# Performance work log

Measured on AMD Instinct MI355X. Metric: run time of the kernel, lower is better.

## Reference

```python
import jax, jax.numpy as jnp
import numpy as np

EPS = 1e-7


def setup_inputs() -> dict:
    key = jax.random.key(0)
    k1, k2, k3 = jax.random.split(key, 3)
    B, Nt, Nv, D = 64, 128, 256, 512
    text_feats = jax.random.normal(k1, (B, Nt, D), dtype=jnp.float32)
    visual_feats = jax.random.normal(k2, (B, Nv, D), dtype=jnp.float32)
    attention_mask = jax.random.randint(k3, (B, Nt), 0, 2, dtype=jnp.int32)
    return {"text_feats": text_feats, "visual_feats": visual_feats,
            "attention_mask": attention_mask}


def _l2norm(x):
    return x / jnp.clip(jnp.linalg.norm(x, axis=-1, keepdims=True), 1e-12)


def reference(text_feats, visual_feats, attention_mask):
    # Normalize token features (F.normalize along D)
    t = _l2norm(text_feats)            # (B, Nt, D)
    v = _l2norm(visual_feats)          # (B, Nv, D)
    # All-pairs token similarities: (B, B, Nt, Nv)
    token_sims = jnp.einsum('itd,jvd->ijtv', t, v)
    # Max over visual tokens -> (B, B, Nt)
    max_sims = jnp.max(token_sims, axis=3)
    # Masked mean over text tokens -> (B, B)
    mask = attention_mask.astype(jnp.float32)[:, None, :]   # (B, 1, Nt) broadcasts over pairs
    masked_sum = jnp.sum(max_sims * mask, axis=2)            # (B, B)
    valid = jnp.clip(jnp.sum(mask, axis=2), EPS)             # (B, 1)
    clip_sims = masked_sum / valid                           # (B, B)
    # Symmetric InfoNCE on the diagonal
    B = clip_sims.shape[0]
    diag = jnp.arange(B)
    losses_t2v = -jax.nn.log_softmax(clip_sims, axis=1)[diag, diag]
    losses_v2t = -jax.nn.log_softmax(clip_sims.T, axis=1)[diag, diag]
    contrastive_loss = jnp.mean(losses_t2v + losses_v2t) / 2.0
    # Regularization: keep negative token sims near zero
    neg_sims = jnp.clip(token_sims, -20.0, 0.0)
    reg_loss = 0.15 * jnp.mean(neg_sims ** 2)
    return contrastive_loss + reg_loss
```

## Files before the change

### kernel.cpp

```cpp
#include <hip/hip_runtime.h>
#include <hip/hip_bf16.h>

#define BB 64
#define NT 128
#define NV 256
#define DD 512
#define BKB 128
#define EPSF 1e-7f

typedef __attribute__((ext_vector_type(8))) int i32x8;
typedef __attribute__((ext_vector_type(4))) int i32x4;
typedef __attribute__((ext_vector_type(4))) float f32x4;

__device__ __forceinline__ void glds16(const uchar* g, uchar* l) {
    __builtin_amdgcn_global_load_lds(
        (const __attribute__((address_space(1))) unsigned int*)g,
        (__attribute__((address_space(3))) unsigned int*)l, 16, 0, 0);
}

__global__ __launch_bounds__(256) void k_normalize(
    const float* __restrict__ tf, const float* __restrict__ vf,
    uchar* __restrict__ tn, uchar* __restrict__ vn,
    float* __restrict__ reg_sum) {
    if (blockIdx.x == 0 && threadIdx.x == 0) *reg_sum = 0.0f;
    const int w = threadIdx.x >> 6, l = threadIdx.x & 63;
    const int row = blockIdx.x * 4 + w;
    const float* src;
    uchar* dst;
    if (row < BB * NT) {
        src = tf + (size_t)row * DD;
        dst = tn + (size_t)row * DD;
    } else {
        int r = row - BB * NT;
        src = vf + (size_t)r * DD;
        dst = vn + (size_t)r * DD;
    }
    float4 x0 = ((const float4*)src)[l * 2];
    float4 x1 = ((const float4*)src)[l * 2 + 1];
    float ss = x0.x * x0.x + x0.y * x0.y + x0.z * x0.z + x0.w * x0.w
             + x1.x * x1.x + x1.y * x1.y + x1.z * x1.z + x1.w * x1.w;
    #pragma unroll
    for (int off = 32; off; off >>= 1) ss += __shfl_xor(ss, off, 64);
    float scale = 1.0f / fmaxf(sqrtf(ss), 1e-12f);
    int p0 = __builtin_amdgcn_cvt_pk_fp8_f32(x0.x * scale, x0.y * scale, 0, 0);
    p0 = __builtin_amdgcn_cvt_pk_fp8_f32(x0.z * scale, x0.w * scale, p0, 1);
    int p1 = __builtin_amdgcn_cvt_pk_fp8_f32(x1.x * scale, x1.y * scale, 0, 0);
    p1 = __builtin_amdgcn_cvt_pk_fp8_f32(x1.z * scale, x1.w * scale, p1, 1);
    ((uint2*)dst)[l] = make_uint2((unsigned)p0, (unsigned)p1);
}

__global__ __launch_bounds__(512, 2) void k_gemm(
    const uchar* __restrict__ tn, const uchar* __restrict__ vn,
    const int* __restrict__ mask,
    float* __restrict__ clip_sims, float* __restrict__ reg_sum) {
    __shared__ uchar sT0[NT * BKB];
    __shared__ uchar sT1[NT * BKB];
    __shared__ uchar sV0[NV * BKB];
    __shared__ uchar sV1[NV * BKB];
    __shared__ float maxbuf[NT][4];
    __shared__ float redw[8];
    __shared__ float c0[2], c1[2];

    const int i = blockIdx.x, j = blockIdx.y;
    const int tid = threadIdx.x;
    const int l = tid & 63, w = tid >> 6;
    const int wr = w >> 2, wc = w & 3;
    const int m15 = l & 15, q = l >> 4;

    const uchar* tbase = tn + (size_t)i * NT * DD;
    const uchar* vbase = vn + (size_t)j * NV * DD;

    int t_off[2], v_off[4];
    #pragma unroll
    for (int s = 0; s < 2; ++s) {
        int f = s * 512 + tid;
        int r = f >> 3, p = f & 7, g = (p - r) & 7;
        t_off[s] = r * DD + g * 16;
    }
    #pragma unroll
    for (int s = 0; s < 4; ++s) {
        int f = s * 512 + tid;
        int r = f >> 3, p = f & 7, g = (p - r) & 7;
        v_off[s] = r * DD + g * 16;
    }

    int a_b0[4], a_b1[4], b_b0[4], b_b1[4];
    #pragma unroll
    for (int rt = 0; rt < 4; ++rt) {
        int row = wr * 64 + rt * 16 + m15;
        a_b0[rt] = row * BKB + (((2 * q + row) & 7) * 16);
        a_b1[rt] = row * BKB + (((2 * q + 1 + row) & 7) * 16);
    }
    #pragma unroll
    for (int ct = 0; ct < 4; ++ct) {
        int row = wc * 64 + ct * 16 + m15;
        b_b0[ct] = row * BKB + (((2 * q + row) & 7) * 16);
        b_b1[ct] = row * BKB + (((2 * q + 1 + row) & 7) * 16);
    }

    f32x4 acc[4][4];
    #pragma unroll
    for (int rt = 0; rt < 4; ++rt)
        #pragma unroll
        for (int ct = 0; ct < 4; ++ct) acc[rt][ct] = (f32x4){0.f, 0.f, 0.f, 0.f};

    auto stage = [&](uchar* dT, uchar* dV, int kk) {
        #pragma unroll
        for (int s = 0; s < 2; ++s)
            glds16(tbase + t_off[s] + kk, dT + (s * 512 + tid) * 16);
        #pragma unroll
        for (int s = 0; s < 4; ++s)
            glds16(vbase + v_off[s] + kk, dV + (s * 512 + tid) * 16);
    };
    auto compute = [&](const uchar* bT, const uchar* bV) {
        i32x8 bf[4];
        #pragma unroll
        for (int ct = 0; ct < 4; ++ct) {
            i32x4 lo = *(const i32x4*)(bV + b_b0[ct]);
            i32x4 hi = *(const i32x4*)(bV + b_b1[ct]);
            bf[ct] = (i32x8){lo.x, lo.y, lo.z, lo.w, hi.x, hi.y, hi.z, hi.w};
        }
        #pragma unroll
        for (int rt = 0; rt < 4; ++rt) {
            i32x4 lo = *(const i32x4*)(bT + a_b0[rt]);
            i32x4 hi = *(const i32x4*)(bT + a_b1[rt]);
            i32x8 a = (i32x8){lo.x, lo.y, lo.z, lo.w, hi.x, hi.y, hi.z, hi.w};
            #pragma unroll
            for (int ct = 0; ct < 4; ++ct)
                acc[rt][ct] = __builtin_amdgcn_mfma_scale_f32_16x16x128_f8f6f4(
                    a, bf[ct], acc[rt][ct],
                    0 , 0 ,
                    0, 127 , 0, 127 );
        }
    };

    stage(sT0, sV0, 0);
    __syncthreads();

    stage(sT1, sV1, 1 * BKB);
    compute(sT0, sV0);
    __syncthreads();

    stage(sT0, sV0, 2 * BKB);
    compute(sT1, sV1);
    __syncthreads();

    stage(sT1, sV1, 3 * BKB);
    compute(sT0, sV0);
    __syncthreads();

    compute(sT1, sV1);

    float rp = 0.0f;
    #pragma unroll
    for (int rt = 0; rt < 4; ++rt)
        #pragma unroll
        for (int ct = 0; ct < 4; ++ct)
            #pragma unroll
            for (int r = 0; r < 4; ++r) {
                float m = fminf(acc[rt][ct][r], 0.0f);
                rp = fmaf(m, m, rp);
            }

    #pragma unroll
    for (int rt = 0; rt < 4; ++rt)
        #pragma unroll
        for (int r = 0; r < 4; ++r) {
            float m = acc[rt][0][r];
            #pragma unroll
            for (int ct = 1; ct < 4; ++ct) m = fmaxf(m, acc[rt][ct][r]);
            #pragma unroll
            for (int msk = 1; msk < 16; msk <<= 1)
                m = fmaxf(m, __shfl_xor(m, msk, 64));
            if (m15 == 0)
                maxbuf[wr * 64 + rt * 16 + q * 4 + r][wc] = m;
        }

    #pragma unroll
    for (int off = 32; off; off >>= 1) rp += __shfl_down(rp, off, 64);
    if (l == 0) redw[w] = rp;
    __syncthreads();

    if (tid < NT) {
        float rm = fmaxf(fmaxf(maxbuf[tid][0], maxbuf[tid][1]),
                         fmaxf(maxbuf[tid][2], maxbuf[tid][3]));
        float mf = (float)mask[i * NT + tid];
        float v = rm * mf;
        #pragma unroll
        for (int off = 32; off; off >>= 1) {
            v += __shfl_down(v, off, 64);
            mf += __shfl_down(mf, off, 64);
        }
        if (l == 0) { c0[w] = v; c1[w] = mf; }
    }
    __syncthreads();
    if (tid == 0) {
        clip_sims[i * BB + j] = (c0[0] + c0[1]) / fmaxf(c1[0] + c1[1], EPSF);
        float s = 0.0f;
        #pragma unroll
        for (int x = 0; x < 8; ++x) s += redw[x];
        atomicAdd(reg_sum, s);
    }
}

__global__ __launch_bounds__(256) void k_loss(
    const float* __restrict__ clip_sims, const float* __restrict__ reg_sum,
    float* __restrict__ out) {
    __shared__ float sc[BB][BB + 1];
    __shared__ float lrow[BB], lcol[BB];
    int tid = threadIdx.x;
    for (int idx = tid; idx < BB * BB; idx += 256)
        sc[idx / BB][idx % BB] = clip_sims[idx];
    __syncthreads();
    if (tid < BB) {
        int i = tid;
        float m = sc[i][0];
        #pragma unroll
        for (int j = 1; j < BB; ++j) m = fmaxf(m, sc[i][j]);
        float s = 0.0f;
        #pragma unroll
        for (int j = 0; j < BB; ++j) s += expf(sc[i][j] - m);
        lrow[i] = m + logf(s) - sc[i][i];
    } else if (tid < 2 * BB) {
        int i = tid - BB;
        float m = sc[0][i];
        #pragma unroll
        for (int j = 1; j < BB; ++j) m = fmaxf(m, sc[j][i]);
        float s = 0.0f;
        #pragma unroll
        for (int j = 0; j < BB; ++j) s += expf(sc[j][i] - m);
        lcol[i] = m + logf(s) - sc[i][i];
    }
    __syncthreads();
    if (tid == 0) {
        float tot = 0.0f;
        for (int i = 0; i < BB; ++i) tot += lrow[i] + lcol[i];
        float contrastive = tot / (2.0f * BB);
        double denom = (double)BB * BB * NT * NV;
        float reg = 0.15f * (float)((double)reg_sum[0] / denom);
        out[0] = contrastive + reg;
    }
}

extern "C" void kernel_launch(void* const* d_in, const int* in_sizes, int n_in,
                              void* d_out, int out_size, void* d_ws, size_t ws_size,
                              hipStream_t stream) {
    const float* tf = (const float*)d_in[0];
    const float* vf = (const float*)d_in[1];
    const int* mask = (const int*)d_in[2];
    float* out = (float*)d_out;

    char* ws = (char*)d_ws;
    size_t tn_bytes = (size_t)BB * NT * DD;
    size_t vn_bytes = (size_t)BB * NV * DD;
    size_t cs_bytes = (size_t)BB * BB * sizeof(float);

    uchar* tn = (uchar*)ws;
    uchar* vn = (uchar*)(ws + tn_bytes);
    float* clip_sims = (float*)(ws + tn_bytes + vn_bytes);
    float* reg_sum = (float*)(ws + tn_bytes + vn_bytes + cs_bytes);

    k_normalize<<<(BB * NT + BB * NV) / 4, 256, 0, stream>>>(tf, vf, tn, vn, reg_sum);
    k_gemm<<<dim3(BB, BB), 512, 0, stream>>>(tn, vn, mask, clip_sims, reg_sum);
    k_loss<<<1, 256, 0, stream>>>(clip_sims, reg_sum, out);
}
```

Measured before the change: 233.1 us.

## Load visual B-operand directly from global, drop its LDS staging, remap blocks per XCD

The visual-token operand is no longer staged through shared memory. Each wave reads its MFMA B fragments straight from global memory, which cuts LDS use from about 96KB to 32KB per block, and launch bounds are raised to allow 4 blocks per CU. The grid is flattened to 1D and block IDs are remapped so that each XCD handles a contiguous set of j (visual) indices, aiming for better L2 reuse of the visual tiles. The trade-off is that B-fragment loads now come from global/L2 latency, are shared by the four row-waves without LDS reuse, and are not prefetched ahead of compute.

```diff
diff --git a/kernel.cpp b/kernel.cpp
--- a/kernel.cpp
+++ b/kernel.cpp
@@ -49,19 +49,22 @@
     ((uint2*)dst)[l] = make_uint2((unsigned)p0, (unsigned)p1);
 }
 
-__global__ __launch_bounds__(512, 2) void k_gemm(
+__global__ __launch_bounds__(512, 4) void k_gemm(
     const uchar* __restrict__ tn, const uchar* __restrict__ vn,
     const int* __restrict__ mask,
     float* __restrict__ clip_sims, float* __restrict__ reg_sum) {
     __shared__ uchar sT0[NT * BKB];
     __shared__ uchar sT1[NT * BKB];
-    __shared__ uchar sV0[NV * BKB];
-    __shared__ uchar sV1[NV * BKB];
     __shared__ float maxbuf[NT][4];
     __shared__ float redw[8];
     __shared__ float c0[2], c1[2];
 
-    const int i = blockIdx.x, j = blockIdx.y;
+    const int bid = blockIdx.x;
+    const int xcd = bid & 7;
+    const int seq = bid >> 3;
+    const int i = seq >> 3;
+    const int j = xcd * 8 + (seq & 7);
+
     const int tid = threadIdx.x;
     const int l = tid & 63, w = tid >> 6;
     const int wr = w >> 2, wc = w & 3;
@@ -70,33 +73,23 @@
     const uchar* tbase = tn + (size_t)i * NT * DD;
     const uchar* vbase = vn + (size_t)j * NV * DD;
 
-    int t_off[2], v_off[4];
+    int t_off[2];
     #pragma unroll
     for (int s = 0; s < 2; ++s) {
         int f = s * 512 + tid;
         int r = f >> 3, p = f & 7, g = (p - r) & 7;
         t_off[s] = r * DD + g * 16;
     }
-    #pragma unroll
-    for (int s = 0; s < 4; ++s) {
-        int f = s * 512 + tid;
-        int r = f >> 3, p = f & 7, g = (p - r) & 7;
-        v_off[s] = r * DD + g * 16;
-    }
-
-    int a_b0[4], a_b1[4], b_b0[4], b_b1[4];
+
+    int a_b0[4], a_b1[4];
     #pragma unroll
     for (int rt = 0; rt < 4; ++rt) {
         int row = wr * 64 + rt * 16 + m15;
         a_b0[rt] = row * BKB + (((2 * q + row) & 7) * 16);
         a_b1[rt] = row * BKB + (((2 * q + 1 + row) & 7) * 16);
     }
-    #pragma unroll
-    for (int ct = 0; ct < 4; ++ct) {
-        int row = wc * 64 + ct * 16 + m15;
-        b_b0[ct] = row * BKB + (((2 * q + row) & 7) * 16);
-        b_b1[ct] = row * BKB + (((2 * q + 1 + row) & 7) * 16);
-    }
+
+    const uchar* vptr = vbase + (size_t)((wc * 64 + m15) * DD + q * 32);
 
     f32x4 acc[4][4];
     #pragma unroll
@@ -104,20 +97,18 @@
         #pragma unroll
         for (int ct = 0; ct < 4; ++ct) acc[rt][ct] = (f32x4){0.f, 0.f, 0.f, 0.f};
 
-    auto stage = [&](uchar* dT, uchar* dV, int kk) {
+    auto stage = [&](uchar* dT, int kk) {
         #pragma unroll
         for (int s = 0; s < 2; ++s)
             glds16(tbase + t_off[s] + kk, dT + (s * 512 + tid) * 16);
-        #pragma unroll
-        for (int s = 0; s < 4; ++s)
-            glds16(vbase + v_off[s] + kk, dV + (s * 512 + tid) * 16);
     };
-    auto compute = [&](const uchar* bT, const uchar* bV) {
+    auto compute = [&](const uchar* bT, int kk) {
         i32x8 bf[4];
         #pragma unroll
         for (int ct = 0; ct < 4; ++ct) {
-            i32x4 lo = *(const i32x4*)(bV + b_b0[ct]);
-            i32x4 hi = *(const i32x4*)(bV + b_b1[ct]);
+            const uchar* vp = vptr + ct * (16 * DD) + kk;
+            i32x4 lo = *(const i32x4*)(vp);
+            i32x4 hi = *(const i32x4*)(vp + 16);
             bf[ct] = (i32x8){lo.x, lo.y, lo.z, lo.w, hi.x, hi.y, hi.z, hi.w};
         }
         #pragma unroll
@@ -134,22 +125,22 @@
         }
     };
 
-    stage(sT0, sV0, 0);
-    __syncthreads();
-
-    stage(sT1, sV1, 1 * BKB);
-    compute(sT0, sV0);
-    __syncthreads();
-
-    stage(sT0, sV0, 2 * BKB);
-    compute(sT1, sV1);
-    __syncthreads();
-
-    stage(sT1, sV1, 3 * BKB);
-    compute(sT0, sV0);
-    __syncthreads();
-
-    compute(sT1, sV1);
+    stage(sT0, 0);
+    __syncthreads();
+
+    stage(sT1, 1 * BKB);
+    compute(sT0, 0);
+    __syncthreads();
+
+    stage(sT0, 2 * BKB);
+    compute(sT1, 1 * BKB);
+    __syncthreads();
+
+    stage(sT1, 3 * BKB);
+    compute(sT0, 2 * BKB);
+    __syncthreads();
+
+    compute(sT1, 3 * BKB);
 
     float rp = 0.0f;
     #pragma unroll
@@ -198,7 +189,7 @@
         clip_sims[i * BB + j] = (c0[0] + c0[1]) / fmaxf(c1[0] + c1[1], EPSF);
         float s = 0.0f;
         #pragma unroll
-        for (int x = 0; x < 8; ++x) s += redw[x];
+        for (int x2 = 0; x2 < 8; ++x2) s += redw[x2];
         atomicAdd(reg_sum, s);
     }
 }
@@ -261,6 +252,6 @@
     float* reg_sum = (float*)(ws + tn_bytes + vn_bytes + cs_bytes);
 
     k_normalize<<<(BB * NT + BB * NV) / 4, 256, 0, stream>>>(tf, vf, tn, vn, reg_sum);
-    k_gemm<<<dim3(BB, BB), 512, 0, stream>>>(tn, vn, mask, clip_sims, reg_sum);
+    k_gemm<<<BB * BB, 512, 0, stream>>>(tn, vn, mask, clip_sims, reg_sum);
     k_loss<<<1, 256, 0, stream>>>(clip_sims, reg_sum, out);
 }
```

New measurement: 737.5 us. 216% more time.

## Load text operand directly from global and remap blocks across XCDs for L2 reuse

Applied to the files above, without the earlier changes.

The text tile is no longer staged through LDS. Each wave reads its A fragments straight from global memory into registers, which removes the sT double buffers and their LDS traffic. The grid becomes 1D and is remapped so that each XCD handles a fixed group of eight visual batches, so visual tiles are reused within that XCD's L2. In exchange, the A loads now go to global memory inside the compute loop without prefetch, so their latency may be exposed, and the freed LDS could raise occupancy.

```diff
diff --git a/kernel.cpp b/kernel.cpp
--- a/kernel.cpp
+++ b/kernel.cpp
@@ -53,15 +53,18 @@
     const uchar* __restrict__ tn, const uchar* __restrict__ vn,
     const int* __restrict__ mask,
     float* __restrict__ clip_sims, float* __restrict__ reg_sum) {
-    __shared__ uchar sT0[NT * BKB];
-    __shared__ uchar sT1[NT * BKB];
     __shared__ uchar sV0[NV * BKB];
     __shared__ uchar sV1[NV * BKB];
     __shared__ float maxbuf[NT][4];
     __shared__ float redw[8];
     __shared__ float c0[2], c1[2];
 
-    const int i = blockIdx.x, j = blockIdx.y;
+    const int bid = blockIdx.x;
+    const int xcd = bid & 7;
+    const int seq = bid >> 3;
+    const int i = seq >> 3;
+    const int j = xcd * 8 + (seq & 7);
+
     const int tid = threadIdx.x;
     const int l = tid & 63, w = tid >> 6;
     const int wr = w >> 2, wc = w & 3;
@@ -70,13 +73,7 @@
     const uchar* tbase = tn + (size_t)i * NT * DD;
     const uchar* vbase = vn + (size_t)j * NV * DD;
 
-    int t_off[2], v_off[4];
-    #pragma unroll
-    for (int s = 0; s < 2; ++s) {
-        int f = s * 512 + tid;
-        int r = f >> 3, p = f & 7, g = (p - r) & 7;
-        t_off[s] = r * DD + g * 16;
-    }
+    int v_off[4];
     #pragma unroll
     for (int s = 0; s < 4; ++s) {
         int f = s * 512 + tid;
@@ -84,13 +81,7 @@
         v_off[s] = r * DD + g * 16;
     }
 
-    int a_b0[4], a_b1[4], b_b0[4], b_b1[4];
-    #pragma unroll
-    for (int rt = 0; rt < 4; ++rt) {
-        int row = wr * 64 + rt * 16 + m15;
-        a_b0[rt] = row * BKB + (((2 * q + row) & 7) * 16);
-        a_b1[rt] = row * BKB + (((2 * q + 1 + row) & 7) * 16);
-    }
+    int b_b0[4], b_b1[4];
     #pragma unroll
     for (int ct = 0; ct < 4; ++ct) {
         int row = wc * 64 + ct * 16 + m15;
@@ -98,21 +89,20 @@
         b_b1[ct] = row * BKB + (((2 * q + 1 + row) & 7) * 16);
     }
 
+    const uchar* tptr = tbase + (size_t)((wr * 64 + m15) * DD + q * 32);
+
     f32x4 acc[4][4];
     #pragma unroll
     for (int rt = 0; rt < 4; ++rt)
         #pragma unroll
         for (int ct = 0; ct < 4; ++ct) acc[rt][ct] = (f32x4){0.f, 0.f, 0.f, 0.f};
 
-    auto stage = [&](uchar* dT, uchar* dV, int kk) {
-        #pragma unroll
-        for (int s = 0; s < 2; ++s)
-            glds16(tbase + t_off[s] + kk, dT + (s * 512 + tid) * 16);
+    auto stage = [&](uchar* dV, int kk) {
         #pragma unroll
         for (int s = 0; s < 4; ++s)
             glds16(vbase + v_off[s] + kk, dV + (s * 512 + tid) * 16);
     };
-    auto compute = [&](const uchar* bT, const uchar* bV) {
+    auto compute = [&](const uchar* bV, int kk) {
         i32x8 bf[4];
         #pragma unroll
         for (int ct = 0; ct < 4; ++ct) {
@@ -122,8 +112,9 @@
         }
         #pragma unroll
         for (int rt = 0; rt < 4; ++rt) {
-            i32x4 lo = *(const i32x4*)(bT + a_b0[rt]);
-            i32x4 hi = *(const i32x4*)(bT + a_b1[rt]);
+            const uchar* tp = tptr + rt * (16 * DD) + kk;
+            i32x4 lo = *(const i32x4*)(tp);
+            i32x4 hi = *(const i32x4*)(tp + 16);
             i32x8 a = (i32x8){lo.x, lo.y, lo.z, lo.w, hi.x, hi.y, hi.z, hi.w};
             #pragma unroll
             for (int ct = 0; ct < 4; ++ct)
@@ -134,22 +125,22 @@
         }
     };
 
-    stage(sT0, sV0, 0);
-    __syncthreads();
-
-    stage(sT1, sV1, 1 * BKB);
-    compute(sT0, sV0);
-    __syncthreads();
-
-    stage(sT0, sV0, 2 * BKB);
-    compute(sT1, sV1);
-    __syncthreads();
-
-    stage(sT1, sV1, 3 * BKB);
-    compute(sT0, sV0);
-    __syncthreads();
-
-    compute(sT1, sV1);
+    stage(sV0, 0);
+    __syncthreads();
+
+    stage(sV1, 1 * BKB);
+    compute(sV0, 0);
+    __syncthreads();
+
+    stage(sV0, 2 * BKB);
+    compute(sV1, 1 * BKB);
+    __syncthreads();
+
+    stage(sV1, 3 * BKB);
+    compute(sV0, 2 * BKB);
+    __syncthreads();
+
+    compute(sV1, 3 * BKB);
 
     float rp = 0.0f;
     #pragma unroll
@@ -198,7 +189,7 @@
         clip_sims[i * BB + j] = (c0[0] + c0[1]) / fmaxf(c1[0] + c1[1], EPSF);
         float s = 0.0f;
         #pragma unroll
-        for (int x = 0; x < 8; ++x) s += redw[x];
+        for (int x2 = 0; x2 < 8; ++x2) s += redw[x2];
         atomicAdd(reg_sum, s);
     }
 }
@@ -261,6 +252,6 @@
     float* reg_sum = (float*)(ws + tn_bytes + vn_bytes + cs_bytes);
 
     k_normalize<<<(BB * NT + BB * NV) / 4, 256, 0, stream>>>(tf, vf, tn, vn, reg_sum);
-    k_gemm<<<dim3(BB, BB), 512, 0, stream>>>(tn, vn, mask, clip_sims, reg_sum);
+    k_gemm<<<BB * BB, 512, 0, stream>>>(tn, vn, mask, clip_sims, reg_sum);
     k_loss<<<1, 256, 0, stream>>>(clip_sims, reg_sum, out);
 }
```

New measurement: 299.8 us. 28.6% more time.

## Split GEMM block into two visual halves with 256 threads and vmcnt-pipelined staging

Applied to the files above, without the earlier changes.

The GEMM block drops from 512 to 256 threads (4 waves). It now covers the 256 visual tokens as two 128-row halves processed one after the other over 8 K-stages. Each half's max and regularization results are flushed into separate maxbuf columns. Staging uses a two-deep prefetch with explicit s_waitcnt vmcnt plus raw barriers instead of __syncthreads, so loads of stage s+2 overlap compute of stage s. This halves the LDS footprint per block, which may allow more resident blocks, at the cost of more serial work per block and reloading the text tile for each half.

```diff
diff --git a/kernel.cpp b/kernel.cpp
--- a/kernel.cpp
+++ b/kernel.cpp
@@ -49,39 +49,34 @@
     ((uint2*)dst)[l] = make_uint2((unsigned)p0, (unsigned)p1);
 }
 
-__global__ __launch_bounds__(512, 2) void k_gemm(
+__global__ __launch_bounds__(256, 2) void k_gemm(
     const uchar* __restrict__ tn, const uchar* __restrict__ vn,
     const int* __restrict__ mask,
     float* __restrict__ clip_sims, float* __restrict__ reg_sum) {
-    __shared__ uchar sT0[NT * BKB];
-    __shared__ uchar sT1[NT * BKB];
-    __shared__ uchar sV0[NV * BKB];
-    __shared__ uchar sV1[NV * BKB];
+    __shared__ uchar sT0[128 * BKB];
+    __shared__ uchar sT1[128 * BKB];
+    __shared__ uchar sV0[128 * BKB];
+    __shared__ uchar sV1[128 * BKB];
     __shared__ float maxbuf[NT][4];
-    __shared__ float redw[8];
+    __shared__ float redw[4];
     __shared__ float c0[2], c1[2];
 
     const int i = blockIdx.x, j = blockIdx.y;
     const int tid = threadIdx.x;
     const int l = tid & 63, w = tid >> 6;
-    const int wr = w >> 2, wc = w & 3;
+    const int wr = w >> 1, wc = w & 1;
     const int m15 = l & 15, q = l >> 4;
 
     const uchar* tbase = tn + (size_t)i * NT * DD;
-    const uchar* vbase = vn + (size_t)j * NV * DD;
-
-    int t_off[2], v_off[4];
-    #pragma unroll
-    for (int s = 0; s < 2; ++s) {
-        int f = s * 512 + tid;
+    const uchar* vb0 = vn + (size_t)j * NV * DD;
+    const uchar* vb1 = vb0 + (size_t)128 * DD;
+
+    int soff[4];
+    #pragma unroll
+    for (int s = 0; s < 4; ++s) {
+        int f = s * 256 + tid;
         int r = f >> 3, p = f & 7, g = (p - r) & 7;
-        t_off[s] = r * DD + g * 16;
-    }
-    #pragma unroll
-    for (int s = 0; s < 4; ++s) {
-        int f = s * 512 + tid;
-        int r = f >> 3, p = f & 7, g = (p - r) & 7;
-        v_off[s] = r * DD + g * 16;
+        soff[s] = r * DD + g * 16;
     }
 
     int a_b0[4], a_b1[4], b_b0[4], b_b1[4];
@@ -103,16 +98,23 @@
     for (int rt = 0; rt < 4; ++rt)
         #pragma unroll
         for (int ct = 0; ct < 4; ++ct) acc[rt][ct] = (f32x4){0.f, 0.f, 0.f, 0.f};
-
-    auto stage = [&](uchar* dT, uchar* dV, int kk) {
-        #pragma unroll
-        for (int s = 0; s < 2; ++s)
-            glds16(tbase + t_off[s] + kk, dT + (s * 512 + tid) * 16);
-        #pragma unroll
-        for (int s = 0; s < 4; ++s)
-            glds16(vbase + v_off[s] + kk, dV + (s * 512 + tid) * 16);
+    float rp = 0.0f;
+
+    auto stage = [&](int s) {
+        uchar* dT = (s & 1) ? sT1 : sT0;
+        uchar* dV = (s & 1) ? sV1 : sV0;
+        const uchar* vb = (s >= 4) ? vb1 : vb0;
+        const int kk = (s & 3) * BKB;
+        #pragma unroll
+        for (int u = 0; u < 4; ++u)
+            glds16(tbase + soff[u] + kk, dT + (u * 256 + tid) * 16);
+        #pragma unroll
+        for (int u = 0; u < 4; ++u)
+            glds16(vb + soff[u] + kk, dV + (u * 256 + tid) * 16);
     };
-    auto compute = [&](const uchar* bT, const uchar* bV) {
+    auto compute = [&](int s) {
+        const uchar* bT = (s & 1) ? sT1 : sT0;
+        const uchar* bV = (s & 1) ? sV1 : sV0;
         i32x8 bf[4];
         #pragma unroll
         for (int ct = 0; ct < 4; ++ct) {
@@ -133,48 +135,50 @@
                     0, 127 , 0, 127 );
         }
     };
-
-    stage(sT0, sV0, 0);
-    __syncthreads();
-
-    stage(sT1, sV1, 1 * BKB);
-    compute(sT0, sV0);
-    __syncthreads();
-
-    stage(sT0, sV0, 2 * BKB);
-    compute(sT1, sV1);
-    __syncthreads();
-
-    stage(sT1, sV1, 3 * BKB);
-    compute(sT0, sV0);
-    __syncthreads();
-
-    compute(sT1, sV1);
-
-    float rp = 0.0f;
-    #pragma unroll
-    for (int rt = 0; rt < 4; ++rt)
-        #pragma unroll
-        for (int ct = 0; ct < 4; ++ct)
+    auto flush = [&](int jh) {
+        #pragma unroll
+        for (int rt = 0; rt < 4; ++rt)
+            #pragma unroll
+            for (int ct = 0; ct < 4; ++ct)
+                #pragma unroll
+                for (int r = 0; r < 4; ++r) {
+                    float m = fminf(acc[rt][ct][r], 0.0f);
+                    rp = fmaf(m, m, rp);
+                }
+        #pragma unroll
+        for (int rt = 0; rt < 4; ++rt)
             #pragma unroll
             for (int r = 0; r < 4; ++r) {
-                float m = fminf(acc[rt][ct][r], 0.0f);
-                rp = fmaf(m, m, rp);
+                float m = acc[rt][0][r];
+                #pragma unroll
+                for (int ct = 1; ct < 4; ++ct) m = fmaxf(m, acc[rt][ct][r]);
+                #pragma unroll
+                for (int msk = 1; msk < 16; msk <<= 1)
+                    m = fmaxf(m, __shfl_xor(m, msk, 64));
+                if (m15 == 0)
+                    maxbuf[wr * 64 + rt * 16 + q * 4 + r][wc * 2 + jh] = m;
             }
-
-    #pragma unroll
-    for (int rt = 0; rt < 4; ++rt)
-        #pragma unroll
-        for (int r = 0; r < 4; ++r) {
-            float m = acc[rt][0][r];
-            #pragma unroll
-            for (int ct = 1; ct < 4; ++ct) m = fmaxf(m, acc[rt][ct][r]);
-            #pragma unroll
-            for (int msk = 1; msk < 16; msk <<= 1)
-                m = fmaxf(m, __shfl_xor(m, msk, 64));
-            if (m15 == 0)
-                maxbuf[wr * 64 + rt * 16 + q * 4 + r][wc] = m;
-        }
+        #pragma unroll
+        for (int rt = 0; rt < 4; ++rt)
+            #pragma unroll
+            for (int ct = 0; ct < 4; ++ct) acc[rt][ct] = (f32x4){0.f, 0.f, 0.f, 0.f};
+    };
+
+    stage(0);
+    stage(1);
+    #pragma unroll
+    for (int s = 0; s < 8; ++s) {
+        if (s < 7) { asm volatile("s_waitcnt vmcnt(8)" ::: "memory"); }
+        else       { asm volatile("s_waitcnt vmcnt(0)" ::: "memory"); }
+        __builtin_amdgcn_s_barrier();
+        asm volatile("" ::: "memory");
+        compute(s);
+        if (s == 3) flush(0);
+        if (s == 7) flush(1);
+        asm volatile("" ::: "memory");
+        __builtin_amdgcn_s_barrier();
+        if (s + 2 < 8) stage(s + 2);
+    }
 
     #pragma unroll
     for (int off = 32; off; off >>= 1) rp += __shfl_down(rp, off, 64);
@@ -196,9 +200,7 @@
     __syncthreads();
     if (tid == 0) {
         clip_sims[i * BB + j] = (c0[0] + c0[1]) / fmaxf(c1[0] + c1[1], EPSF);
-        float s = 0.0f;
-        #pragma unroll
-        for (int x = 0; x < 8; ++x) s += redw[x];
+        float s = redw[0] + redw[1] + redw[2] + redw[3];
         atomicAdd(reg_sum, s);
     }
 }
@@ -261,6 +263,6 @@
     float* reg_sum = (float*)(ws + tn_bytes + vn_bytes + cs_bytes);
 
     k_normalize<<<(BB * NT + BB * NV) / 4, 256, 0, stream>>>(tf, vf, tn, vn, reg_sum);
-    k_gemm<<<dim3(BB, BB), 512, 0, stream>>>(tn, vn, mask, clip_sims, reg_sum);
+    k_gemm<<<dim3(BB, BB), 256, 0, stream>>>(tn, vn, mask, clip_sims, reg_sum);
     k_loss<<<1, 256, 0, stream>>>(clip_sims, reg_sum, out);
 }
```

Measured after the change: 416.2 us. +78.6%, slower.
